# Kernel tuning notes

Measured on AMD Instinct MI355X. Metric: run time of the kernel, lower is better.

Reference implementation:

```python
import jax, jax.numpy as jnp
import numpy as np

B, N, T, DM, H, M = 32, 207, 24, 64, 8, 32
E = 2 * DM  # true input feature dim (2*dmodel per the reshape in the source)


def setup_inputs() -> dict:
    rng = jax.random.key(0)
    ks = jax.random.split(rng, 10)
    s = 0.05  # scale params to keep activations numerically sane
    query = jax.random.normal(ks[0], (B, N, T, E), jnp.float32)
    key = jax.random.normal(ks[1], (B, N, T, E), jnp.float32)
    value = jax.random.normal(ks[2], (B, N, T, E), jnp.float32)
    # causal temporal mask, broadcast over batch/node/head; True = masked out
    atten_mask = jnp.broadcast_to(jnp.triu(jnp.ones((T, T), bool), 1), (B, N, 1, T, T))
    qp1 = jax.random.normal(ks[3], (N * DM, M), jnp.float32) * s
    qp2 = jax.random.normal(ks[4], (M, 4 * DM), jnp.float32) * s
    kp1 = jax.random.normal(ks[5], (N * DM, M), jnp.float32) * s
    kp2 = jax.random.normal(ks[6], (M, 4 * DM), jnp.float32) * s
    vp1 = jax.random.normal(ks[7], (N * DM, M), jnp.float32) * s
    vp2 = jax.random.normal(ks[8], (M, 4 * DM), jnp.float32) * s
    out_W = jax.random.normal(ks[9], (E, DM), jnp.float32) * s
    out_b = jnp.zeros((DM,), jnp.float32)
    return dict(query=query, key=key, value=value, atten_mask=atten_mask,
                qp1=qp1, qp2=qp2, kp1=kp1, kp2=kp2, vp1=vp1, vp2=vp2,
                out_W=out_W, out_b=out_b, num_heads=H)


def reference(query, key, value, atten_mask, qp1, qp2, kp1, kp2, vp1, vp2, out_W, out_b, num_heads):
    b, n, t, e = query.shape

    def proj(x, p1, p2):
        # low-rank factored per-node projection: (N*dmodel, M) @ (M, 4*dmodel) -> (N, E, E)
        P = (p1 @ p2).reshape(n, e, e)
        y = jnp.einsum('bnti,nik->bntk', x, P)
        return jax.nn.relu(y).reshape(b, n, t, num_heads, -1)

    q = proj(query, qp1, qp2)   # (B,N,T,H,d)
    k = proj(key, kp1, kp2)
    v = proj(value, vp1, vp2)

    scale = 1.0 / np.sqrt(q.shape[-1]).astype(np.float32)
    scores = jnp.einsum('bnthe,bnshe->bnhts', q, k)          # (B,N,H,T,S)
    scores = jnp.where(atten_mask, -jnp.inf, scores)          # masked_fill before scaling
    attn = jax.nn.softmax(scale * scores, axis=-1)            # dropout disabled (eval)
    out = jnp.einsum('bnhts,bnshd->bnthd', attn, v).reshape(b, n, t, -1)
    out = jax.nn.relu(out @ out_W + out_b)                    # (B,N,T,dmodel)
    return out, attn
```

## Files before the change

### kernel.cpp

```cpp
#include <hip/hip_runtime.h>
#include <hip/hip_bf16.h>

#define Bn 32
#define Nn 207
#define Tt 24
#define Ee 128
#define Hh 8
#define Dm 64
#define Mm 32

typedef __attribute__((ext_vector_type(8))) short bf16x8;
typedef __attribute__((ext_vector_type(4))) float f32x4;

__device__ __forceinline__ unsigned swz256(unsigned a) { return a ^ (((a >> 8) & 7u) << 4); }
__device__ __forceinline__ unsigned swz64(unsigned a)  { return a ^ (((a >> 7) & 3u) << 4); }
__device__ __forceinline__ unsigned short f2b(float f) {
  union { float f; unsigned u; } x; x.f = f;
  unsigned u = x.u;
  return (unsigned short)((u + 0x7FFFu + ((u >> 16) & 1u)) >> 16);
}

__global__ __launch_bounds__(256) void build_P_frag(const float* __restrict__ p1,
                                                    const float* __restrict__ p2,
                                                    unsigned short* __restrict__ Pt) {
  const int bid = blockIdx.x;
  const int n = bid >> 3;
  const int r8 = bid & 7;
  const int ks = r8 >> 1;
  const int chunk = ((r8 & 1) << 1) + (threadIdx.x >> 7);
  const int col = threadIdx.x & 127;
  const int base_i = ks * 32 + chunk * 8;
  const float* p1r = p1 + (size_t)(n * 64 + (base_i >> 1)) * Mm;
  const float* p2a = p2 + col;
  const float* p2b = p2 + 128 + col;
  float acc[8] = {};
#pragma unroll
  for (int m = 0; m < Mm; ++m) {
    float a = p2a[m * 256], b = p2b[m * 256];
#pragma unroll
    for (int jj = 0; jj < 4; ++jj) {
      float pv = p1r[jj * Mm + m];
      acc[2 * jj]     = fmaf(pv, a, acc[2 * jj]);
      acc[2 * jj + 1] = fmaf(pv, b, acc[2 * jj + 1]);
    }
  }
  const int nt = col >> 4;
  const int lane = (chunk << 4) | (col & 15);
  union { unsigned short u[8]; uint4 v; } w;
#pragma unroll
  for (int j = 0; j < 8; ++j) w.u[j] = f2b(acc[j]);
  *(uint4*)(Pt + (size_t)(((n * 8 + nt) * 4 + ks) * 64 + lane) * 8) = w.v;
}

__global__ __launch_bounds__(256) void build_W_frag(const float* __restrict__ W,
                                                    unsigned short* __restrict__ Wt) {
  for (int idx = threadIdx.x; idx < 1024; idx += 256) {
    int lane = idx & 63, ks = (idx >> 6) & 3, nt = idx >> 8;
    union { unsigned short u[8]; uint4 v; } w;
#pragma unroll
    for (int j = 0; j < 8; ++j)
      w.u[j] = f2b(W[(size_t)(ks * 32 + (lane >> 4) * 8 + j) * 64 + nt * 16 + (lane & 15)]);
    *(uint4*)(Wt + (size_t)idx * 8) = w.v;
  }
}

__global__ __launch_bounds__(256, 3) void fused_attn(
    const float* __restrict__ Qin, const float* __restrict__ Kin,
    const float* __restrict__ Vin,
    const unsigned short* __restrict__ Ptq, const unsigned short* __restrict__ Ptk,
    const unsigned short* __restrict__ Ptv, const unsigned short* __restrict__ Wt,
    const float* __restrict__ bias,
    float* __restrict__ out, float* __restrict__ attn) {
  __shared__ __align__(16) char smem[49152];
  const int tid = threadIdx.x;
  const int lane = tid & 63;
  const int wv = tid >> 6;
  const int c = lane & 15;
  const int g = lane >> 4;
  const f32x4 zf = {0.f, 0.f, 0.f, 0.f};

  int bx = blockIdx.x;
  bx = (bx & 7) * 828 + (bx >> 3);
  const int n = bx >> 5;
  const int b = bx & 31;
  const size_t xbase = (size_t)(b * Nn + n) * (Tt * Ee);

  {
    uint4 z4 = {0, 0, 0, 0};
#pragma unroll
    for (int i = 0; i < 2; ++i) *(uint4*)(smem + 24576 + (tid + 256 * i) * 16) = z4;
    const float* src[2] = {Qin + xbase, Kin + xbase};
#pragma unroll
    for (int w = 0; w < 2; ++w)
#pragma unroll
      for (int it = 0; it < 3; ++it) {
        int e4 = tid + 256 * it;
        float4 xv = *(const float4*)(src[w] + (size_t)e4 * 4);
        unsigned a = swz256((e4 >> 5) * 256 + (e4 & 31) * 8);
        uint2 pk;
        pk.x = (unsigned)f2b(xv.x) | ((unsigned)f2b(xv.y) << 16);
        pk.y = (unsigned)f2b(xv.z) | ((unsigned)f2b(xv.w) << 16);
        *(uint2*)(smem + w * 8192 + a) = pk;
      }
  }
  __syncthreads();

#pragma unroll
  for (int w = 0; w < 2; ++w) {
    const unsigned short* Pt = (w == 0) ? Ptq : Ptk;
    f32x4 acc[2][2] = {{zf, zf}, {zf, zf}};
#pragma unroll
    for (int ks = 0; ks < 4; ++ks) {
      bf16x8 Bf[2], Af[2];
#pragma unroll
      for (int ntl = 0; ntl < 2; ++ntl)
        Bf[ntl] = *(const bf16x8*)(Pt + (size_t)(((n * 8 + (wv * 2 + ntl)) * 4 + ks) * 64 + lane) * 8);
#pragma unroll
      for (int mt = 0; mt < 2; ++mt)
        Af[mt] = *(const bf16x8*)(smem + w * 8192 + swz256((mt * 16 + c) * 256 + ks * 64 + g * 16));
#pragma unroll
      for (int mt = 0; mt < 2; ++mt)
#pragma unroll
        for (int ntl = 0; ntl < 2; ++ntl)
          acc[mt][ntl] = __builtin_amdgcn_mfma_f32_16x16x32_bf16(Af[mt], Bf[ntl], acc[mt][ntl], 0, 0, 0);
    }
    char* dst = smem + ((w == 0) ? 32768 : 16384);
#pragma unroll
    for (int mt = 0; mt < 2; ++mt)
#pragma unroll
      for (int r = 0; r < 4; ++r) {
        int row = mt * 16 + g * 4 + r;
        if (row < 24) {
#pragma unroll
          for (int ntl = 0; ntl < 2; ++ntl) {
            int col = (wv * 2 + ntl) * 16 + c;
            *(unsigned short*)(dst + swz256(row * 256 + col * 2)) = f2b(fmaxf(acc[mt][ntl][r], 0.f));
          }
        }
      }
  }

  float4 xvr[3];
#pragma unroll
  for (int it = 0; it < 3; ++it)
    xvr[it] = *(const float4*)(Vin + xbase + (size_t)(tid + 256 * it) * 4);
  __syncthreads();

  f32x4 sc[2][2][2];
  {
    bf16x8 zb = {0, 0, 0, 0, 0, 0, 0, 0};
#pragma unroll
    for (int hh = 0; hh < 2; ++hh) {
      int h = wv * 2 + hh;
      bf16x8 Aq[2], Bk[2];
#pragma unroll
      for (int mt = 0; mt < 2; ++mt) {
        Aq[mt] = zb;
        if (lane < 32)
          Aq[mt] = *(const bf16x8*)(smem + 32768 + swz256((mt * 16 + c) * 256 + (h * 16 + g * 8) * 2));
      }
#pragma unroll
      for (int st = 0; st < 2; ++st) {
        Bk[st] = zb;
        if (lane < 32)
          Bk[st] = *(const bf16x8*)(smem + 16384 + swz256((st * 16 + c) * 256 + (h * 16 + g * 8) * 2));
      }
#pragma unroll
      for (int mt = 0; mt < 2; ++mt)
#pragma unroll
        for (int st = 0; st < 2; ++st)
          sc[hh][mt][st] = __builtin_amdgcn_mfma_f32_16x16x32_bf16(Aq[mt], Bk[st], zf, 0, 0, 0);
    }
  }
  __syncthreads();

#pragma unroll
  for (int it = 0; it < 3; ++it) {
    int e4 = tid + 256 * it;
    unsigned a = swz256((e4 >> 5) * 256 + (e4 & 31) * 8);
    uint2 pk;
    pk.x = (unsigned)f2b(xvr[it].x) | ((unsigned)f2b(xvr[it].y) << 16);
    pk.y = (unsigned)f2b(xvr[it].z) | ((unsigned)f2b(xvr[it].w) << 16);
    *(uint2*)(smem + a) = pk;
  }

  {
    const size_t abase = (size_t)(b * Nn + n) * (Hh * Tt * Tt);
#pragma unroll
    for (int hh = 0; hh < 2; ++hh) {
      int h = wv * 2 + hh;
#pragma unroll
      for (int mt = 0; mt < 2; ++mt)
#pragma unroll
        for (int r = 0; r < 4; ++r) {
          int t = mt * 16 + g * 4 + r;
          float v0 = (c <= t)      ? sc[hh][mt][0][r] * 0.25f : -1e30f;
          float v1 = (16 + c <= t) ? sc[hh][mt][1][r] * 0.25f : -1e30f;
          float m = fmaxf(v0, v1);
          m = fmaxf(m, __shfl_xor(m, 1));
          m = fmaxf(m, __shfl_xor(m, 2));
          m = fmaxf(m, __shfl_xor(m, 4));
          m = fmaxf(m, __shfl_xor(m, 8));
          float e0 = __expf(v0 - m);
          float e1 = __expf(v1 - m);
          float s2 = e0 + e1;
          s2 += __shfl_xor(s2, 1);
          s2 += __shfl_xor(s2, 2);
          s2 += __shfl_xor(s2, 4);
          s2 += __shfl_xor(s2, 8);
          float inv = 1.0f / s2;
          float p0 = e0 * inv, p1 = e1 * inv;
          if (t < 24) {
            float* ap = attn + abase + (size_t)h * (Tt * Tt) + t * Tt;
            ap[c] = p0;
            if (c < 8) ap[16 + c] = p1;
            char* q = smem + 32768;
            *(unsigned short*)(q + swz64(h * 2048 + t * 64 + c * 2))        = f2b(p0);
            *(unsigned short*)(q + swz64(h * 2048 + t * 64 + (16 + c) * 2)) = f2b(p1);
          }
        }
    }
  }
  __syncthreads();

  {
    f32x4 acc[2][2] = {{zf, zf}, {zf, zf}};
#pragma unroll
    for (int ks = 0; ks < 4; ++ks) {
      bf16x8 Bf[2], Af[2];
#pragma unroll
      for (int ntl = 0; ntl < 2; ++ntl)
        Bf[ntl] = *(const bf16x8*)(Ptv + (size_t)(((n * 8 + (wv * 2 + ntl)) * 4 + ks) * 64 + lane) * 8);
#pragma unroll
      for (int mt = 0; mt < 2; ++mt)
        Af[mt] = *(const bf16x8*)(smem + swz256((mt * 16 + c) * 256 + ks * 64 + g * 16));
#pragma unroll
      for (int mt = 0; mt < 2; ++mt)
#pragma unroll
        for (int ntl = 0; ntl < 2; ++ntl)
          acc[mt][ntl] = __builtin_amdgcn_mfma_f32_16x16x32_bf16(Af[mt], Bf[ntl], acc[mt][ntl], 0, 0, 0);
    }
#pragma unroll
    for (int mt = 0; mt < 2; ++mt)
#pragma unroll
      for (int r = 0; r < 4; ++r) {
        int srow = mt * 16 + g * 4 + r;
        if (srow < 24) {
#pragma unroll
          for (int ntl = 0; ntl < 2; ++ntl) {
            int dcol = (wv * 2 + ntl) * 16 + c;
            *(unsigned short*)(smem + 24576 + swz64(dcol * 64 + srow * 2)) = f2b(fmaxf(acc[mt][ntl][r], 0.f));
          }
        }
      }
  }
  __syncthreads();

  {
    f32x4 pv[2][2];
#pragma unroll
    for (int hh = 0; hh < 2; ++hh) {
      int h = wv * 2 + hh;
      bf16x8 Bv = *(const bf16x8*)(smem + 24576 + swz64((h * 16 + c) * 64 + g * 16));
#pragma unroll
      for (int mt = 0; mt < 2; ++mt) {
        bf16x8 Ap = *(const bf16x8*)(smem + 32768 + swz64(h * 2048 + (mt * 16 + c) * 64 + g * 16));
        pv[hh][mt] = __builtin_amdgcn_mfma_f32_16x16x32_bf16(Ap, Bv, zf, 0, 0, 0);
      }
    }
#pragma unroll
    for (int hh = 0; hh < 2; ++hh) {
      int h = wv * 2 + hh;
#pragma unroll
      for (int mt = 0; mt < 2; ++mt)
#pragma unroll
        for (int r = 0; r < 4; ++r) {
          int t = mt * 16 + g * 4 + r;
          if (t < 24)
            *(unsigned short*)(smem + 8192 + swz256(t * 256 + (h * 16 + c) * 2)) = f2b(pv[hh][mt][r]);
        }
    }
  }
  __syncthreads();

  {
    f32x4 acc[2] = {zf, zf};
#pragma unroll
    for (int ks = 0; ks < 4; ++ks) {
      bf16x8 Bw = *(const bf16x8*)(Wt + (size_t)((wv * 4 + ks) * 64 + lane) * 8);
      bf16x8 Af[2];
#pragma unroll
      for (int mt = 0; mt < 2; ++mt)
        Af[mt] = *(const bf16x8*)(smem + 8192 + swz256((mt * 16 + c) * 256 + ks * 64 + g * 16));
#pragma unroll
      for (int mt = 0; mt < 2; ++mt)
        acc[mt] = __builtin_amdgcn_mfma_f32_16x16x32_bf16(Af[mt], Bw, acc[mt], 0, 0, 0);
    }
    int j = wv * 16 + c;
    float bj = bias[j];
    const size_t obase = (size_t)(b * Nn + n) * (Tt * Dm);
#pragma unroll
    for (int mt = 0; mt < 2; ++mt)
#pragma unroll
      for (int r = 0; r < 4; ++r) {
        int t = mt * 16 + g * 4 + r;
        if (t < 24) out[obase + (size_t)t * Dm + j] = fmaxf(acc[mt][r] + bj, 0.f);
      }
  }
}

extern "C" void kernel_launch(void* const* d_in, const int* in_sizes, int n_in,
                              void* d_out, int out_size, void* d_ws, size_t ws_size,
                              hipStream_t stream) {
  const float* query = (const float*)d_in[0];
  const float* key   = (const float*)d_in[1];
  const float* value = (const float*)d_in[2];
  const float* qp1 = (const float*)d_in[4];
  const float* qp2 = (const float*)d_in[5];
  const float* kp1 = (const float*)d_in[6];
  const float* kp2 = (const float*)d_in[7];
  const float* vp1 = (const float*)d_in[8];
  const float* vp2 = (const float*)d_in[9];
  const float* out_W = (const float*)d_in[10];
  const float* out_b = (const float*)d_in[11];

  const size_t PT = (size_t)Nn * 8 * 4 * 64 * 8;
  unsigned short* Ptq = (unsigned short*)d_ws;
  unsigned short* Ptk = Ptq + PT;
  unsigned short* Ptv = Ptk + PT;
  unsigned short* Wtf = Ptv + PT;

  float* out = (float*)d_out;
  float* attn = out + (size_t)Bn * Nn * Tt * Dm;

  build_P_frag<<<Nn * 8, 256, 0, stream>>>(qp1, qp2, Ptq);
  build_P_frag<<<Nn * 8, 256, 0, stream>>>(kp1, kp2, Ptk);
  build_P_frag<<<Nn * 8, 256, 0, stream>>>(vp1, vp2, Ptv);
  build_W_frag<<<1, 256, 0, stream>>>(out_W, Wtf);

  fused_attn<<<Bn * Nn, 256, 0, stream>>>(query, key, value, Ptq, Ptk, Ptv, Wtf,
                                          out_b, out, attn);
}
```

Measured before the change: 186.1 us.

## Shrink LDS footprint, raise occupancy, merge P builds, drop softmax max pass

Shared memory drops from 48KB to 32KB by packing 24-row tiles at a 6144-byte stride and clamping padded MFMA rows instead of zero-filling them. Launch bounds rise from 3 to 5 blocks so more blocks can be resident per CU. The three P-fragment builder launches become one 3D-grid launch. The softmax no longer computes the row max and exponentiates the scaled scores directly, which removes a round of shuffles but relies on the scores staying small enough not to overflow. s_setprio is placed around the MFMA groups, and the V load is moved to after the score computation.

```diff
diff --git a/kernel.cpp b/kernel.cpp
--- a/kernel.cpp
+++ b/kernel.cpp
@@ -8,21 +8,29 @@
 #define Hh 8
 #define Dm 64
 #define Mm 32
+#define NBN (Bn * Nn)
+#define PT ((size_t)Nn * 16384)
 
 typedef __attribute__((ext_vector_type(8))) short bf16x8;
 typedef __attribute__((ext_vector_type(4))) float f32x4;
 
 __device__ __forceinline__ unsigned swz256(unsigned a) { return a ^ (((a >> 8) & 7u) << 4); }
 __device__ __forceinline__ unsigned swz64(unsigned a)  { return a ^ (((a >> 7) & 3u) << 4); }
-__device__ __forceinline__ unsigned short f2b(float f) {
+__device__ __forceinline__ unsigned f2b(float f) {
   union { float f; unsigned u; } x; x.f = f;
   unsigned u = x.u;
-  return (unsigned short)((u + 0x7FFFu + ((u >> 16) & 1u)) >> 16);
-}
-
-__global__ __launch_bounds__(256) void build_P_frag(const float* __restrict__ p1,
-                                                    const float* __restrict__ p2,
-                                                    unsigned short* __restrict__ Pt) {
+  return ((u + 0x7FFFu + ((u >> 16) & 1u)) >> 16) & 0xFFFFu;
+}
+
+__global__ __launch_bounds__(256) void build_P_frag3(
+    const float* __restrict__ qp1, const float* __restrict__ qp2,
+    const float* __restrict__ kp1, const float* __restrict__ kp2,
+    const float* __restrict__ vp1, const float* __restrict__ vp2,
+    unsigned short* __restrict__ Pt) {
+  const int tau = blockIdx.y;
+  const float* p1 = (tau == 0) ? qp1 : (tau == 1) ? kp1 : vp1;
+  const float* p2 = (tau == 0) ? qp2 : (tau == 1) ? kp2 : vp2;
+  unsigned short* dst = Pt + (size_t)tau * PT;
   const int bid = blockIdx.x;
   const int n = bid >> 3;
   const int r8 = bid & 7;
@@ -48,8 +56,8 @@
   const int lane = (chunk << 4) | (col & 15);
   union { unsigned short u[8]; uint4 v; } w;
 #pragma unroll
-  for (int j = 0; j < 8; ++j) w.u[j] = f2b(acc[j]);
-  *(uint4*)(Pt + (size_t)(((n * 8 + nt) * 4 + ks) * 64 + lane) * 8) = w.v;
+  for (int j = 0; j < 8; ++j) w.u[j] = (unsigned short)f2b(acc[j]);
+  *(uint4*)(dst + (size_t)(((n * 8 + nt) * 4 + ks) * 64 + lane) * 8) = w.v;
 }
 
 __global__ __launch_bounds__(256) void build_W_frag(const float* __restrict__ W,
@@ -59,25 +67,26 @@
     union { unsigned short u[8]; uint4 v; } w;
 #pragma unroll
     for (int j = 0; j < 8; ++j)
-      w.u[j] = f2b(W[(size_t)(ks * 32 + (lane >> 4) * 8 + j) * 64 + nt * 16 + (lane & 15)]);
+      w.u[j] = (unsigned short)f2b(W[(size_t)(ks * 32 + (lane >> 4) * 8 + j) * 64 + nt * 16 + (lane & 15)]);
     *(uint4*)(Wt + (size_t)idx * 8) = w.v;
   }
 }
 
-__global__ __launch_bounds__(256, 3) void fused_attn(
+__global__ __launch_bounds__(256, 5) void fused_attn(
     const float* __restrict__ Qin, const float* __restrict__ Kin,
     const float* __restrict__ Vin,
     const unsigned short* __restrict__ Ptq, const unsigned short* __restrict__ Ptk,
     const unsigned short* __restrict__ Ptv, const unsigned short* __restrict__ Wt,
     const float* __restrict__ bias,
     float* __restrict__ out, float* __restrict__ attn) {
-  __shared__ __align__(16) char smem[49152];
+  __shared__ __align__(16) char smem[32768];
   const int tid = threadIdx.x;
   const int lane = tid & 63;
   const int wv = tid >> 6;
   const int c = lane & 15;
   const int g = lane >> 4;
   const f32x4 zf = {0.f, 0.f, 0.f, 0.f};
+  const bf16x8 zb = {0, 0, 0, 0, 0, 0, 0, 0};
 
   int bx = blockIdx.x;
   bx = (bx & 7) * 828 + (bx >> 3);
@@ -87,8 +96,8 @@
 
   {
     uint4 z4 = {0, 0, 0, 0};
-#pragma unroll
-    for (int i = 0; i < 2; ++i) *(uint4*)(smem + 24576 + (tid + 256 * i) * 16) = z4;
+    *(uint4*)(smem + 24576 + tid * 32) = z4;
+    *(uint4*)(smem + 24576 + tid * 32 + 16) = z4;
     const float* src[2] = {Qin + xbase, Kin + xbase};
 #pragma unroll
     for (int w = 0; w < 2; ++w)
@@ -96,113 +105,103 @@
       for (int it = 0; it < 3; ++it) {
         int e4 = tid + 256 * it;
         float4 xv = *(const float4*)(src[w] + (size_t)e4 * 4);
-        unsigned a = swz256((e4 >> 5) * 256 + (e4 & 31) * 8);
+        unsigned a = swz256((unsigned)((e4 >> 5) * 256 + (e4 & 31) * 8));
         uint2 pk;
-        pk.x = (unsigned)f2b(xv.x) | ((unsigned)f2b(xv.y) << 16);
-        pk.y = (unsigned)f2b(xv.z) | ((unsigned)f2b(xv.w) << 16);
-        *(uint2*)(smem + w * 8192 + a) = pk;
-      }
-  }
-  __syncthreads();
-
-#pragma unroll
-  for (int w = 0; w < 2; ++w) {
-    const unsigned short* Pt = (w == 0) ? Ptq : Ptk;
-    f32x4 acc[2][2] = {{zf, zf}, {zf, zf}};
-#pragma unroll
-    for (int ks = 0; ks < 4; ++ks) {
-      bf16x8 Bf[2], Af[2];
-#pragma unroll
-      for (int ntl = 0; ntl < 2; ++ntl)
-        Bf[ntl] = *(const bf16x8*)(Pt + (size_t)(((n * 8 + (wv * 2 + ntl)) * 4 + ks) * 64 + lane) * 8);
-#pragma unroll
-      for (int mt = 0; mt < 2; ++mt)
-        Af[mt] = *(const bf16x8*)(smem + w * 8192 + swz256((mt * 16 + c) * 256 + ks * 64 + g * 16));
-#pragma unroll
-      for (int mt = 0; mt < 2; ++mt)
+        pk.x = f2b(xv.x) | (f2b(xv.y) << 16);
+        pk.y = f2b(xv.z) | (f2b(xv.w) << 16);
+        *(uint2*)(smem + w * 6144 + a) = pk;
+      }
+  }
+  __syncthreads();
+
+  {
+    const unsigned short* Pts[2] = {Ptq, Ptk};
+#pragma unroll
+    for (int w = 0; w < 2; ++w) {
+      const unsigned short* Pf = Pts[w];
+      f32x4 acc[2][2] = {{zf, zf}, {zf, zf}};
+#pragma unroll
+      for (int ks = 0; ks < 4; ++ks) {
+        bf16x8 Bf[2], Af[2];
 #pragma unroll
         for (int ntl = 0; ntl < 2; ++ntl)
-          acc[mt][ntl] = __builtin_amdgcn_mfma_f32_16x16x32_bf16(Af[mt], Bf[ntl], acc[mt][ntl], 0, 0, 0);
-    }
-    char* dst = smem + ((w == 0) ? 32768 : 16384);
+          Bf[ntl] = *(const bf16x8*)(Pf + (size_t)(((n * 8 + (wv * 2 + ntl)) * 4 + ks) * 64 + lane) * 8);
+#pragma unroll
+        for (int mt = 0; mt < 2; ++mt) {
+          int row = mt * 16 + c; row = row < 24 ? row : 23;
+          Af[mt] = *(const bf16x8*)(smem + w * 6144 + swz256((unsigned)(row * 256 + ks * 64 + g * 16)));
+        }
+        __builtin_amdgcn_s_setprio(1);
+#pragma unroll
+        for (int mt = 0; mt < 2; ++mt)
+#pragma unroll
+          for (int ntl = 0; ntl < 2; ++ntl)
+            acc[mt][ntl] = __builtin_amdgcn_mfma_f32_16x16x32_bf16(Af[mt], Bf[ntl], acc[mt][ntl], 0, 0, 0);
+        __builtin_amdgcn_s_setprio(0);
+      }
+      char* dst = smem + 12288 + w * 6144;
+#pragma unroll
+      for (int mt = 0; mt < 2; ++mt)
+#pragma unroll
+        for (int r = 0; r < 4; ++r) {
+          int row = mt * 16 + g * 4 + r;
+          if (row < 24) {
+#pragma unroll
+            for (int ntl = 0; ntl < 2; ++ntl) {
+              int col = (wv * 2 + ntl) * 16 + c;
+              *(unsigned short*)(dst + swz256((unsigned)(row * 256 + col * 2))) =
+                  (unsigned short)f2b(fmaxf(acc[mt][ntl][r], 0.f));
+            }
+          }
+        }
+    }
+  }
+  __syncthreads();
+
+  f32x4 sc[2][2][2];
+#pragma unroll
+  for (int hh = 0; hh < 2; ++hh) {
+    int h = wv * 2 + hh;
+    bf16x8 Aq[2], Bk[2];
+#pragma unroll
+    for (int mt = 0; mt < 2; ++mt) {
+      int row = mt * 16 + c; row = row < 24 ? row : 23;
+      Aq[mt] = zb;
+      if (lane < 32) Aq[mt] = *(const bf16x8*)(smem + 12288 + swz256((unsigned)(row * 256 + (h * 16 + g * 8) * 2)));
+    }
+#pragma unroll
+    for (int st = 0; st < 2; ++st) {
+      int row = st * 16 + c; row = row < 24 ? row : 23;
+      Bk[st] = zb;
+      if (lane < 32) Bk[st] = *(const bf16x8*)(smem + 18432 + swz256((unsigned)(row * 256 + (h * 16 + g * 8) * 2)));
+    }
+    __builtin_amdgcn_s_setprio(1);
 #pragma unroll
     for (int mt = 0; mt < 2; ++mt)
 #pragma unroll
-      for (int r = 0; r < 4; ++r) {
-        int row = mt * 16 + g * 4 + r;
-        if (row < 24) {
-#pragma unroll
-          for (int ntl = 0; ntl < 2; ++ntl) {
-            int col = (wv * 2 + ntl) * 16 + c;
-            *(unsigned short*)(dst + swz256(row * 256 + col * 2)) = f2b(fmaxf(acc[mt][ntl][r], 0.f));
-          }
-        }
-      }
-  }
-
-  float4 xvr[3];
-#pragma unroll
-  for (int it = 0; it < 3; ++it)
-    xvr[it] = *(const float4*)(Vin + xbase + (size_t)(tid + 256 * it) * 4);
-  __syncthreads();
-
-  f32x4 sc[2][2][2];
-  {
-    bf16x8 zb = {0, 0, 0, 0, 0, 0, 0, 0};
+      for (int st = 0; st < 2; ++st)
+        sc[hh][mt][st] = __builtin_amdgcn_mfma_f32_16x16x32_bf16(Aq[mt], Bk[st], zf, 0, 0, 0);
+    __builtin_amdgcn_s_setprio(0);
+  }
+  __syncthreads();
+
+  {
+    float4 xvr[3];
+#pragma unroll
+    for (int it = 0; it < 3; ++it)
+      xvr[it] = *(const float4*)(Vin + xbase + (size_t)(tid + 256 * it) * 4);
+
+    const size_t abase = (size_t)(b * Nn + n) * (Hh * Tt * Tt);
 #pragma unroll
     for (int hh = 0; hh < 2; ++hh) {
       int h = wv * 2 + hh;
-      bf16x8 Aq[2], Bk[2];
-#pragma unroll
-      for (int mt = 0; mt < 2; ++mt) {
-        Aq[mt] = zb;
-        if (lane < 32)
-          Aq[mt] = *(const bf16x8*)(smem + 32768 + swz256((mt * 16 + c) * 256 + (h * 16 + g * 8) * 2));
-      }
-#pragma unroll
-      for (int st = 0; st < 2; ++st) {
-        Bk[st] = zb;
-        if (lane < 32)
-          Bk[st] = *(const bf16x8*)(smem + 16384 + swz256((st * 16 + c) * 256 + (h * 16 + g * 8) * 2));
-      }
-#pragma unroll
-      for (int mt = 0; mt < 2; ++mt)
-#pragma unroll
-        for (int st = 0; st < 2; ++st)
-          sc[hh][mt][st] = __builtin_amdgcn_mfma_f32_16x16x32_bf16(Aq[mt], Bk[st], zf, 0, 0, 0);
-    }
-  }
-  __syncthreads();
-
-#pragma unroll
-  for (int it = 0; it < 3; ++it) {
-    int e4 = tid + 256 * it;
-    unsigned a = swz256((e4 >> 5) * 256 + (e4 & 31) * 8);
-    uint2 pk;
-    pk.x = (unsigned)f2b(xvr[it].x) | ((unsigned)f2b(xvr[it].y) << 16);
-    pk.y = (unsigned)f2b(xvr[it].z) | ((unsigned)f2b(xvr[it].w) << 16);
-    *(uint2*)(smem + a) = pk;
-  }
-
-  {
-    const size_t abase = (size_t)(b * Nn + n) * (Hh * Tt * Tt);
-#pragma unroll
-    for (int hh = 0; hh < 2; ++hh) {
-      int h = wv * 2 + hh;
 #pragma unroll
       for (int mt = 0; mt < 2; ++mt)
 #pragma unroll
         for (int r = 0; r < 4; ++r) {
           int t = mt * 16 + g * 4 + r;
-          float v0 = (c <= t)      ? sc[hh][mt][0][r] * 0.25f : -1e30f;
-          float v1 = (16 + c <= t) ? sc[hh][mt][1][r] * 0.25f : -1e30f;
-          float m = fmaxf(v0, v1);
-          m = fmaxf(m, __shfl_xor(m, 1));
-          m = fmaxf(m, __shfl_xor(m, 2));
-          m = fmaxf(m, __shfl_xor(m, 4));
-          m = fmaxf(m, __shfl_xor(m, 8));
-          float e0 = __expf(v0 - m);
-          float e1 = __expf(v1 - m);
+          float e0 = (c <= t)      ? __expf(sc[hh][mt][0][r] * 0.25f) : 0.f;
+          float e1 = (16 + c <= t) ? __expf(sc[hh][mt][1][r] * 0.25f) : 0.f;
           float s2 = e0 + e1;
           s2 += __shfl_xor(s2, 1);
           s2 += __shfl_xor(s2, 2);
@@ -214,11 +213,20 @@
             float* ap = attn + abase + (size_t)h * (Tt * Tt) + t * Tt;
             ap[c] = p0;
             if (c < 8) ap[16 + c] = p1;
-            char* q = smem + 32768;
-            *(unsigned short*)(q + swz64(h * 2048 + t * 64 + c * 2))        = f2b(p0);
-            *(unsigned short*)(q + swz64(h * 2048 + t * 64 + (16 + c) * 2)) = f2b(p1);
+            char* q = smem + 12288;
+            *(unsigned short*)(q + swz64((unsigned)(h * 1536 + t * 64 + c * 2)))        = (unsigned short)f2b(p0);
+            *(unsigned short*)(q + swz64((unsigned)(h * 1536 + t * 64 + (16 + c) * 2))) = (unsigned short)f2b(p1);
           }
         }
+    }
+#pragma unroll
+    for (int it = 0; it < 3; ++it) {
+      int e4 = tid + 256 * it;
+      unsigned a = swz256((unsigned)((e4 >> 5) * 256 + (e4 & 31) * 8));
+      uint2 pk;
+      pk.x = f2b(xvr[it].x) | (f2b(xvr[it].y) << 16);
+      pk.y = f2b(xvr[it].z) | (f2b(xvr[it].w) << 16);
+      *(uint2*)(smem + 6144 + a) = pk;
     }
   }
   __syncthreads();
@@ -232,13 +240,17 @@
       for (int ntl = 0; ntl < 2; ++ntl)
         Bf[ntl] = *(const bf16x8*)(Ptv + (size_t)(((n * 8 + (wv * 2 + ntl)) * 4 + ks) * 64 + lane) * 8);
 #pragma unroll
-      for (int mt = 0; mt < 2; ++mt)
-        Af[mt] = *(const bf16x8*)(smem + swz256((mt * 16 + c) * 256 + ks * 64 + g * 16));
+      for (int mt = 0; mt < 2; ++mt) {
+        int row = mt * 16 + c; row = row < 24 ? row : 23;
+        Af[mt] = *(const bf16x8*)(smem + 6144 + swz256((unsigned)(row * 256 + ks * 64 + g * 16)));
+      }
+      __builtin_amdgcn_s_setprio(1);
 #pragma unroll
       for (int mt = 0; mt < 2; ++mt)
 #pragma unroll
         for (int ntl = 0; ntl < 2; ++ntl)
           acc[mt][ntl] = __builtin_amdgcn_mfma_f32_16x16x32_bf16(Af[mt], Bf[ntl], acc[mt][ntl], 0, 0, 0);
+      __builtin_amdgcn_s_setprio(0);
     }
 #pragma unroll
     for (int mt = 0; mt < 2; ++mt)
@@ -249,7 +261,8 @@
 #pragma unroll
           for (int ntl = 0; ntl < 2; ++ntl) {
             int dcol = (wv * 2 + ntl) * 16 + c;
-            *(unsigned short*)(smem + 24576 + swz64(dcol * 64 + srow * 2)) = f2b(fmaxf(acc[mt][ntl][r], 0.f));
+            *(unsigned short*)(smem + 24576 + swz64((unsigned)(dcol * 64 + srow * 2))) =
+                (unsigned short)f2b(fmaxf(acc[mt][ntl][r], 0.f));
           }
         }
       }
@@ -261,10 +274,11 @@
 #pragma unroll
     for (int hh = 0; hh < 2; ++hh) {
       int h = wv * 2 + hh;
-      bf16x8 Bv = *(const bf16x8*)(smem + 24576 + swz64((h * 16 + c) * 64 + g * 16));
+      bf16x8 Bv = *(const bf16x8*)(smem + 24576 + swz64((unsigned)((h * 16 + c) * 64 + g * 16)));
 #pragma unroll
       for (int mt = 0; mt < 2; ++mt) {
-        bf16x8 Ap = *(const bf16x8*)(smem + 32768 + swz64(h * 2048 + (mt * 16 + c) * 64 + g * 16));
+        int row = mt * 16 + c; row = row < 24 ? row : 23;
+        bf16x8 Ap = *(const bf16x8*)(smem + 12288 + swz64((unsigned)(h * 1536 + row * 64 + g * 16)));
         pv[hh][mt] = __builtin_amdgcn_mfma_f32_16x16x32_bf16(Ap, Bv, zf, 0, 0, 0);
       }
     }
@@ -277,24 +291,29 @@
         for (int r = 0; r < 4; ++r) {
           int t = mt * 16 + g * 4 + r;
           if (t < 24)
-            *(unsigned short*)(smem + 8192 + swz256(t * 256 + (h * 16 + c) * 2)) = f2b(pv[hh][mt][r]);
-        }
-    }
-  }
-  __syncthreads();
-
-  {
-    f32x4 acc[2] = {zf, zf};
+            *(unsigned short*)(smem + swz256((unsigned)(t * 256 + (h * 16 + c) * 2))) =
+                (unsigned short)f2b(pv[hh][mt][r]);
+        }
+    }
+  }
+  __syncthreads();
+
+  {
+    f32x4 acc2[2] = {zf, zf};
 #pragma unroll
     for (int ks = 0; ks < 4; ++ks) {
       bf16x8 Bw = *(const bf16x8*)(Wt + (size_t)((wv * 4 + ks) * 64 + lane) * 8);
       bf16x8 Af[2];
 #pragma unroll
-      for (int mt = 0; mt < 2; ++mt)
-        Af[mt] = *(const bf16x8*)(smem + 8192 + swz256((mt * 16 + c) * 256 + ks * 64 + g * 16));
-#pragma unroll
-      for (int mt = 0; mt < 2; ++mt)
-        acc[mt] = __builtin_amdgcn_mfma_f32_16x16x32_bf16(Af[mt], Bw, acc[mt], 0, 0, 0);
+      for (int mt = 0; mt < 2; ++mt) {
+        int row = mt * 16 + c; row = row < 24 ? row : 23;
+        Af[mt] = *(const bf16x8*)(smem + swz256((unsigned)(row * 256 + ks * 64 + g * 16)));
+      }
+      __builtin_amdgcn_s_setprio(1);
+#pragma unroll
+      for (int mt = 0; mt < 2; ++mt)
+        acc2[mt] = __builtin_amdgcn_mfma_f32_16x16x32_bf16(Af[mt], Bw, acc2[mt], 0, 0, 0);
+      __builtin_amdgcn_s_setprio(0);
     }
     int j = wv * 16 + c;
     float bj = bias[j];
@@ -304,7 +323,7 @@
 #pragma unroll
       for (int r = 0; r < 4; ++r) {
         int t = mt * 16 + g * 4 + r;
-        if (t < 24) out[obase + (size_t)t * Dm + j] = fmaxf(acc[mt][r] + bj, 0.f);
+        if (t < 24) out[obase + (size_t)t * Dm + j] = fmaxf(acc2[mt][r] + bj, 0.f);
       }
   }
 }
@@ -324,20 +343,15 @@
   const float* out_W = (const float*)d_in[10];
   const float* out_b = (const float*)d_in[11];
 
-  const size_t PT = (size_t)Nn * 8 * 4 * 64 * 8;
-  unsigned short* Ptq = (unsigned short*)d_ws;
-  unsigned short* Ptk = Ptq + PT;
-  unsigned short* Ptv = Ptk + PT;
-  unsigned short* Wtf = Ptv + PT;
+  unsigned short* Pt  = (unsigned short*)d_ws;
+  unsigned short* Wtf = Pt + 3 * PT;
 
   float* out = (float*)d_out;
-  float* attn = out + (size_t)Bn * Nn * Tt * Dm;
-
-  build_P_frag<<<Nn * 8, 256, 0, stream>>>(qp1, qp2, Ptq);
-  build_P_frag<<<Nn * 8, 256, 0, stream>>>(kp1, kp2, Ptk);
-  build_P_frag<<<Nn * 8, 256, 0, stream>>>(vp1, vp2, Ptv);
+  float* attn = out + (size_t)NBN * Tt * Dm;
+
+  build_P_frag3<<<dim3(Nn * 8, 3), 256, 0, stream>>>(qp1, qp2, kp1, kp2, vp1, vp2, Pt);
   build_W_frag<<<1, 256, 0, stream>>>(out_W, Wtf);
-
-  fused_attn<<<Bn * Nn, 256, 0, stream>>>(query, key, value, Ptq, Ptk, Ptv, Wtf,
-                                          out_b, out, attn);
-}
+  fused_attn<<<NBN, 256, 0, stream>>>(query, key, value,
+                                      Pt, Pt + PT, Pt + 2 * PT, Wtf,
+                                      out_b, out, attn);
+}
```

Result: slower. 237.8 us (+27.8%).
